# Optimization experiments

Hardware: AMD Instinct MI355X
Metric: run time of the kernel (lower is better)

The kernel has to match this reference:

```python
import jax, jax.numpy as jnp
import numpy as np

# Plain-RNN variant of RNNX (output_sizes=None): 2 stacked Elman layers,
# per layer: h' = tanh(Linear(concat(x, h))). batch_first=False -> Xt is [T, B, I].
T, B, I, H = 512, 128, 256, 512


def setup_inputs() -> dict:
    key = jax.random.key(0)
    k0, k1, k2, k3, k4 = jax.random.split(key, 5)
    stdv = 1.0 / np.sqrt(H)  # reset_parameters: uniform(-1/sqrt(hs), 1/sqrt(hs))
    return {
        "Xt": jax.random.normal(k0, (T, B, I), dtype=jnp.float32),
        "W1": jax.random.uniform(k1, (I + H, H), dtype=jnp.float32, minval=-stdv, maxval=stdv),
        "b1": jax.random.uniform(k2, (H,), dtype=jnp.float32, minval=-stdv, maxval=stdv),
        "W2": jax.random.uniform(k3, (H + H, H), dtype=jnp.float32, minval=-stdv, maxval=stdv),
        "b2": jax.random.uniform(k4, (H,), dtype=jnp.float32, minval=-stdv, maxval=stdv),
    }


def reference(Xt, W1, b1, W2, b2):
    # Xt: [T, B, I]; returns (out [T, B, H] stacked layer-2 outputs, hidden [2, B, H])
    Bsz = Xt.shape[1]
    Hd = W1.shape[1]
    h0 = (jnp.zeros((Bsz, Hd), Xt.dtype), jnp.zeros((Bsz, Hd), Xt.dtype))

    def step(h, x_t):
        h1, h2 = h
        y1 = jnp.tanh(jnp.concatenate([x_t, h1], axis=-1) @ W1 + b1)  # layer 1
        y2 = jnp.tanh(jnp.concatenate([y1, h2], axis=-1) @ W2 + b2)   # layer 2
        return (y1, y2), y2

    (h1f, h2f), out = jax.lax.scan(step, h0, Xt)
    hidden = jnp.stack([h1f, h2f], axis=0)  # [n_layers, B, H]
    return out, hidden
```

## Files before the change

kernel.cpp:

```cpp
#include <hip/hip_runtime.h>
#include <hip/hip_bf16.h>

#define TT 512
#define BB 128
#define II 256
#define HH 512

#define NGROUP 8
#define WPG    16
#define NWG    (NGROUP * WPG)

typedef __attribute__((ext_vector_type(8))) unsigned short ushort8;
typedef __attribute__((ext_vector_type(8))) __bf16         bf16x8;
typedef __attribute__((ext_vector_type(4))) float          float4v;
typedef unsigned long long u64;

union frag8 { ushort8 u; bf16x8 b; u64 q[2]; };

__device__ __forceinline__ unsigned short f2bf(float f) {
    union { float f; unsigned u; } v; v.f = f;
    return (unsigned short)((v.u + 0x7FFFu + ((v.u >> 16) & 1u)) >> 16);
}
__device__ __forceinline__ float bf2f(unsigned short h) {
    union { unsigned u; float f; } v; v.u = ((unsigned)h) << 16;
    return v.f;
}
__device__ __forceinline__ float tanh_fast(float x) {
    float e = __expf(2.0f * x);
    return 1.0f - 2.0f / (e + 1.0f);
}
__device__ __forceinline__ float4v mfma(bf16x8 a, bf16x8 b, float4v c) {
    return __builtin_amdgcn_mfma_f32_16x16x32_bf16(a, b, c, 0, 0, 0);
}
__device__ __forceinline__ u64 ald(const unsigned short* p) {
    return __hip_atomic_load((u64*)(void*)p, __ATOMIC_RELAXED, __HIP_MEMORY_SCOPE_AGENT);
}
__device__ __forceinline__ void ast(unsigned short* p, u64 v) {
    __hip_atomic_store((u64*)(void*)p, v, __ATOMIC_RELAXED, __HIP_MEMORY_SCOPE_AGENT);
}

__global__ __launch_bounds__(256, 1) void rnn_fused(
    const float* __restrict__ Xt,
    const float* __restrict__ W1,
    const float* __restrict__ b1,
    const float* __restrict__ W2,
    const float* __restrict__ b2,
    float* __restrict__ out,
    unsigned short* __restrict__ Ybuf,
    unsigned int* __restrict__ cnt)
{
    const int wg  = blockIdx.x;
    const int g   = wg & 7;
    const int j   = wg >> 3;
    const int tid = threadIdx.x;
    const int w   = tid >> 6;
    const int c   = w & 1;
    const int kh  = w >> 1;
    const int l   = tid & 63;
    const int lr  = l & 15;
    const int lq  = l >> 4;
    const int n0  = j * 32 + c * 16;
    const int row0 = g * 16;

    unsigned short* Y1 = Ybuf;
    unsigned short* Y2 = Ybuf + 2 * BB * HH;

    __shared__ float lp1[2][64][4];
    __shared__ float lp2[2][64][4];
    __shared__ __align__(8) unsigned short tr[4][16][20];

    frag8 w1h[12], w1l[12], w2h[16], w2l[16];
    const int kb1 = kh * 12, kb2 = kh * 16;
#pragma unroll
    for (int q = 0; q < 12; ++q)
#pragma unroll
        for (int e = 0; e < 8; ++e) {
            float v = W1[((kb1 + q) * 32 + lq * 8 + e) * HH + n0 + lr];
            unsigned short hi = f2bf(v);
            w1h[q].u[e] = hi;
            w1l[q].u[e] = f2bf(v - bf2f(hi));
        }
#pragma unroll
    for (int q = 0; q < 16; ++q)
#pragma unroll
        for (int e = 0; e < 8; ++e) {
            float v = W2[((kb2 + q) * 32 + lq * 8 + e) * HH + n0 + lr];
            unsigned short hi = f2bf(v);
            w2h[q].u[e] = hi;
            w2l[q].u[e] = f2bf(v - bf2f(hi));
        }
    const float bias1 = b1[n0 + lr];
    const float bias2 = b2[n0 + lr];

#pragma unroll 1
    for (int t = 0; t <= TT; ++t) {
        const int par = t & 1;
        const unsigned short* y1r = Y1 + (par ^ 1) * (BB * HH);
        const unsigned short* y2r = Y2 + par * (BB * HH);
        unsigned short* y1w = Y1 + par * (BB * HH);
        unsigned short* y2w = Y2 + (par ^ 1) * (BB * HH);

        frag8 a1[16], a2[16];
        if (kh == 0) {
#pragma unroll
            for (int q = 0; q < 16; ++q) {
                const unsigned short* p = y1r + (row0 + lr) * HH + q * 32 + lq * 8;
                a1[q].q[0] = ald(p); a1[q].q[1] = ald(p + 4);
            }
        } else {
#pragma unroll
            for (int q = 4; q < 16; ++q) {
                const unsigned short* p = y1r + (row0 + lr) * HH + q * 32 + lq * 8;
                a1[q].q[0] = ald(p); a1[q].q[1] = ald(p + 4);
            }
            if (t >= 1) {
#pragma unroll
                for (int q = 0; q < 16; ++q) {
                    const unsigned short* p = y2r + (row0 + lr) * HH + q * 32 + lq * 8;
                    a2[q].q[0] = ald(p); a2[q].q[1] = ald(p + 4);
                }
            }
        }

        float4v acc1  = {bias1, bias1, bias1, bias1};
        float4v acc1b = {0.f, 0.f, 0.f, 0.f};
        float4v acc2  = {bias2, bias2, bias2, bias2};
        float4v acc2b = {0.f, 0.f, 0.f, 0.f};
        if (kh == 0) acc2 = acc1b;
        else         acc1 = acc1b;

        if (kh == 0) {
            if (t < TT) {
#pragma unroll
                for (int q = 0; q < 8; ++q) {
                    const float* xp = Xt + ((size_t)t * BB + row0 + lr) * II + q * 32 + lq * 8;
                    float4v x0 = *(const float4v*)xp;
                    float4v x1 = *(const float4v*)(xp + 4);
                    frag8 ax;
#pragma unroll
                    for (int e = 0; e < 4; ++e) { ax.u[e] = f2bf(x0[e]); ax.u[4 + e] = f2bf(x1[e]); }
                    acc1  = mfma(ax.b, w1h[q].b, acc1);
                    acc1b = mfma(ax.b, w1l[q].b, acc1b);
                }
#pragma unroll
                for (int q = 0; q < 4; ++q) {
                    acc1  = mfma(a1[q].b, w1h[8 + q].b, acc1);
                    acc1b = mfma(a1[q].b, w1l[8 + q].b, acc1b);
                }
            }
            if (t >= 1) {
#pragma unroll
                for (int q = 0; q < 16; ++q) {
                    acc2  = mfma(a1[q].b, w2h[q].b, acc2);
                    acc2b = mfma(a1[q].b, w2l[q].b, acc2b);
                }
            }
        } else {
            if (t < TT) {
#pragma unroll
                for (int q = 0; q < 12; ++q) {
                    acc1  = mfma(a1[4 + q].b, w1h[q].b, acc1);
                    acc1b = mfma(a1[4 + q].b, w1l[q].b, acc1b);
                }
            }
            if (t >= 1) {
#pragma unroll
                for (int q = 0; q < 16; ++q) {
                    acc2  = mfma(a2[q].b, w2h[q].b, acc2);
                    acc2b = mfma(a2[q].b, w2l[q].b, acc2b);
                }
            }
        }

        if (kh == 1 && t < TT)  *(float4v*)&lp1[c][l][0] = acc1 + acc1b;
        if (kh == 0 && t >= 1)  *(float4v*)&lp2[c][l][0] = acc2 + acc2b;
        __syncthreads();

        float yout[4];
        if (kh == 0 && t < TT) {
            float4v p = *(const float4v*)&lp1[c][l][0];
#pragma unroll
            for (int i = 0; i < 4; ++i) {
                float y = tanh_fast(acc1[i] + acc1b[i] + p[i]);
                tr[w][lq * 4 + i][lr] = f2bf(y);
                yout[i] = y;
            }
        }
        if (kh == 1 && t >= 1) {
            float4v p = *(const float4v*)&lp2[c][l][0];
#pragma unroll
            for (int i = 0; i < 4; ++i) {
                float y = tanh_fast(acc2[i] + acc2b[i] + p[i]);
                tr[w][lq * 4 + i][lr] = f2bf(y);
                yout[i] = y;
            }
        }
        {
            const int row = l & 15, ch = l >> 4;
            if (kh == 0 && t < TT) {
                u64 v = *(const u64*)&tr[w][row][ch * 4];
                ast(y1w + (row0 + row) * HH + n0 + ch * 4, v);
            }
            if (kh == 1 && t >= 1) {
                u64 v = *(const u64*)&tr[w][row][ch * 4];
                ast(y2w + (row0 + row) * HH + n0 + ch * 4, v);
            }
        }

        asm volatile("s_waitcnt vmcnt(0) lgkmcnt(0)" ::: "memory");
        __syncthreads();

        if (t < TT && tid == 0)
            __hip_atomic_fetch_add(cnt + g * 1024 + t, 1u, __ATOMIC_RELAXED,
                                   __HIP_MEMORY_SCOPE_AGENT);

        if (kh == 1 && t >= 1) {
#pragma unroll
            for (int i = 0; i < 4; ++i) {
                const int r = row0 + lq * 4 + i;
                __builtin_nontemporal_store(yout[i], &out[((size_t)(t - 1) * BB + r) * HH + n0 + lr]);
                if (t == TT)
                    __builtin_nontemporal_store(yout[i],
                        &out[(size_t)TT * BB * HH + (size_t)BB * HH + (size_t)r * HH + n0 + lr]);
            }
        }
        if (kh == 0 && t == TT - 1) {
#pragma unroll
            for (int i = 0; i < 4; ++i) {
                const int r = row0 + lq * 4 + i;
                __builtin_nontemporal_store(yout[i],
                    &out[(size_t)TT * BB * HH + (size_t)r * HH + n0 + lr]);
            }
        }

        if (t < TT) {
            if (tid == 0) {
                while (__hip_atomic_load(cnt + g * 1024 + t, __ATOMIC_RELAXED,
                                         __HIP_MEMORY_SCOPE_AGENT) < WPG)
                    __builtin_amdgcn_s_sleep(1);
            }
            __syncthreads();
        }
    }
}

extern "C" void kernel_launch(void* const* d_in, const int* in_sizes, int n_in,
                              void* d_out, int out_size, void* d_ws, size_t ws_size,
                              hipStream_t stream) {
    const float* Xt = (const float*)d_in[0];
    const float* W1 = (const float*)d_in[1];
    const float* b1 = (const float*)d_in[2];
    const float* W2 = (const float*)d_in[3];
    const float* b2 = (const float*)d_in[4];
    float* out = (float*)d_out;

    unsigned short* Ybuf = (unsigned short*)d_ws;
    unsigned int*   cnt  = (unsigned int*)((char*)d_ws + 4 * BB * HH * 2);
    size_t zero_bytes = (size_t)4 * BB * HH * 2 + (size_t)NGROUP * 1024 * 4;

    hipMemsetAsync(d_ws, 0, zero_bytes, stream);
    hipLaunchKernelGGL(rnn_fused, dim3(NWG), dim3(256), 0, stream,
                       Xt, W1, b1, W2, b2, out, Ybuf, cnt);
}
```

Measured before the change: 5.468 ms.

## Replace group counter barrier with per-wave flags and prefetch X into LDS

Each step previously ended with a workgroup barrier, a single atomic counter increment per group and a thread-0 spin. That is replaced by per-wave step flags: every wave publishes its own flag and then polls all flags in its group with one wavefront vote, which removes the extra __syncthreads and the serialized spin. The next timestep's X rows are prefetched into a double-buffered LDS area with asynchronous global-to-LDS loads, so X reads come off the critical path. Layer-2 output stores are also deferred by one step so they leave the recurrence tail. The risks are busy-wait traffic on shared flags and subtle cross-wave ordering of the LDS buffers, which now relies on the flag protocol.

```diff
diff --git a/kernel.cpp b/kernel.cpp
--- a/kernel.cpp
+++ b/kernel.cpp
@@ -1,5 +1,4 @@
 #include <hip/hip_runtime.h>
-#include <hip/hip_bf16.h>
 
 #define TT 512
 #define BB 128
@@ -33,10 +32,16 @@
     return __builtin_amdgcn_mfma_f32_16x16x32_bf16(a, b, c, 0, 0, 0);
 }
 __device__ __forceinline__ u64 ald(const unsigned short* p) {
-    return __hip_atomic_load((u64*)(void*)p, __ATOMIC_RELAXED, __HIP_MEMORY_SCOPE_AGENT);
+    return __hip_atomic_load((const u64*)(const void*)p, __ATOMIC_RELAXED, __HIP_MEMORY_SCOPE_AGENT);
 }
 __device__ __forceinline__ void ast(unsigned short* p, u64 v) {
     __hip_atomic_store((u64*)(void*)p, v, __ATOMIC_RELAXED, __HIP_MEMORY_SCOPE_AGENT);
+}
+__device__ __forceinline__ unsigned ald32(const unsigned* p) {
+    return __hip_atomic_load(p, __ATOMIC_RELAXED, __HIP_MEMORY_SCOPE_AGENT);
+}
+__device__ __forceinline__ void ast32(unsigned* p, unsigned v) {
+    __hip_atomic_store(p, v, __ATOMIC_RELAXED, __HIP_MEMORY_SCOPE_AGENT);
 }
 
 __global__ __launch_bounds__(256, 1) void rnn_fused(
@@ -47,7 +52,7 @@
     const float* __restrict__ b2,
     float* __restrict__ out,
     unsigned short* __restrict__ Ybuf,
-    unsigned int* __restrict__ cnt)
+    unsigned* __restrict__ slots)
 {
     const int wg  = blockIdx.x;
     const int g   = wg & 7;
@@ -61,10 +66,12 @@
     const int lq  = l >> 4;
     const int n0  = j * 32 + c * 16;
     const int row0 = g * 16;
+    const int mywave = j * 4 + w;
 
     unsigned short* Y1 = Ybuf;
     unsigned short* Y2 = Ybuf + 2 * BB * HH;
 
+    __shared__ float xlds[2][16][256];
     __shared__ float lp1[2][64][4];
     __shared__ float lp2[2][64][4];
     __shared__ __align__(8) unsigned short tr[4][16][20];
@@ -91,6 +98,20 @@
         }
     const float bias1 = b1[n0 + lr];
     const float bias2 = b2[n0 + lr];
+
+    if (w < 2) {
+#pragma unroll
+        for (int i = 0; i < 8; ++i) {
+            int ci = w * 8 + i;
+            const float* gs = Xt + ((size_t)0 * BB + row0 + ci) * II + l * 4;
+            __builtin_amdgcn_global_load_lds(
+                (const __attribute__((address_space(1))) void*)gs,
+                (__attribute__((address_space(3))) void*)&xlds[0][ci][0], 16, 0, 0);
+        }
+    }
+    __syncthreads();
+
+    float yprev[4] = {0.f, 0.f, 0.f, 0.f};
 
 #pragma unroll 1
     for (int t = 0; t <= TT; ++t) {
@@ -100,6 +121,15 @@
         unsigned short* y1w = Y1 + par * (BB * HH);
         unsigned short* y2w = Y2 + (par ^ 1) * (BB * HH);
 
+        if (kh == 1 && t >= 2) {
+#pragma unroll
+            for (int i = 0; i < 4; ++i) {
+                const int r = row0 + lq * 4 + i;
+                __builtin_nontemporal_store(yprev[i],
+                    &out[((size_t)(t - 2) * BB + r) * HH + n0 + lr]);
+            }
+        }
+
         frag8 a1[16], a2[16];
         if (kh == 0) {
 #pragma unroll
@@ -122,20 +152,31 @@
             }
         }
 
-        float4v acc1  = {bias1, bias1, bias1, bias1};
+        if (w < 2 && t < TT - 1) {
+#pragma unroll
+            for (int i = 0; i < 8; ++i) {
+                int ci = w * 8 + i;
+                const float* gs = Xt + ((size_t)(t + 1) * BB + row0 + ci) * II + l * 4;
+                __builtin_amdgcn_global_load_lds(
+                    (const __attribute__((address_space(1))) void*)gs,
+                    (__attribute__((address_space(3))) void*)&xlds[par ^ 1][ci][0], 16, 0, 0);
+            }
+        }
+
+        float4v acc1  = {0.f, 0.f, 0.f, 0.f};
         float4v acc1b = {0.f, 0.f, 0.f, 0.f};
-        float4v acc2  = {bias2, bias2, bias2, bias2};
+        float4v acc2  = {0.f, 0.f, 0.f, 0.f};
         float4v acc2b = {0.f, 0.f, 0.f, 0.f};
-        if (kh == 0) acc2 = acc1b;
-        else         acc1 = acc1b;
+        if (kh == 0) { acc1[0] = acc1[1] = acc1[2] = acc1[3] = bias1; }
+        else         { acc2[0] = acc2[1] = acc2[2] = acc2[3] = bias2; }
 
         if (kh == 0) {
             if (t < TT) {
 #pragma unroll
                 for (int q = 0; q < 8; ++q) {
-                    const float* xp = Xt + ((size_t)t * BB + row0 + lr) * II + q * 32 + lq * 8;
-                    float4v x0 = *(const float4v*)xp;
-                    float4v x1 = *(const float4v*)(xp + 4);
+                    const float* xr = &xlds[par][lr][q * 32 + lq * 8];
+                    float4v x0 = *(const float4v*)xr;
+                    float4v x1 = *(const float4v*)(xr + 4);
                     frag8 ax;
 #pragma unroll
                     for (int e = 0; e < 4; ++e) { ax.u[e] = f2bf(x0[e]); ax.u[4 + e] = f2bf(x1[e]); }
@@ -176,15 +217,21 @@
         if (kh == 0 && t >= 1)  *(float4v*)&lp2[c][l][0] = acc2 + acc2b;
         __syncthreads();
 
-        float yout[4];
         if (kh == 0 && t < TT) {
             float4v p = *(const float4v*)&lp1[c][l][0];
+            float yv[4];
 #pragma unroll
             for (int i = 0; i < 4; ++i) {
-                float y = tanh_fast(acc1[i] + acc1b[i] + p[i]);
-                tr[w][lq * 4 + i][lr] = f2bf(y);
-                yout[i] = y;
-            }
+                yv[i] = tanh_fast(acc1[i] + acc1b[i] + p[i]);
+                tr[w][lq * 4 + i][lr] = f2bf(yv[i]);
+            }
+            if (t == TT - 1) {
+#pragma unroll
+                for (int i = 0; i < 4; ++i)
+                    out[(size_t)TT * BB * HH + (size_t)(row0 + lq * 4 + i) * HH + n0 + lr] = yv[i];
+            }
+            u64 v = *(const u64*)&tr[w][lr][lq * 4];
+            ast(y1w + (row0 + lr) * HH + n0 + lq * 4, v);
         }
         if (kh == 1 && t >= 1) {
             float4v p = *(const float4v*)&lp2[c][l][0];
@@ -192,54 +239,27 @@
             for (int i = 0; i < 4; ++i) {
                 float y = tanh_fast(acc2[i] + acc2b[i] + p[i]);
                 tr[w][lq * 4 + i][lr] = f2bf(y);
-                yout[i] = y;
-            }
-        }
-        {
-            const int row = l & 15, ch = l >> 4;
-            if (kh == 0 && t < TT) {
-                u64 v = *(const u64*)&tr[w][row][ch * 4];
-                ast(y1w + (row0 + row) * HH + n0 + ch * 4, v);
-            }
-            if (kh == 1 && t >= 1) {
-                u64 v = *(const u64*)&tr[w][row][ch * 4];
-                ast(y2w + (row0 + row) * HH + n0 + ch * 4, v);
-            }
-        }
-
-        asm volatile("s_waitcnt vmcnt(0) lgkmcnt(0)" ::: "memory");
-        __syncthreads();
-
-        if (t < TT && tid == 0)
-            __hip_atomic_fetch_add(cnt + g * 1024 + t, 1u, __ATOMIC_RELAXED,
-                                   __HIP_MEMORY_SCOPE_AGENT);
-
-        if (kh == 1 && t >= 1) {
-#pragma unroll
-            for (int i = 0; i < 4; ++i) {
-                const int r = row0 + lq * 4 + i;
-                __builtin_nontemporal_store(yout[i], &out[((size_t)(t - 1) * BB + r) * HH + n0 + lr]);
-                if (t == TT)
-                    __builtin_nontemporal_store(yout[i],
-                        &out[(size_t)TT * BB * HH + (size_t)BB * HH + (size_t)r * HH + n0 + lr]);
-            }
-        }
-        if (kh == 0 && t == TT - 1) {
-#pragma unroll
-            for (int i = 0; i < 4; ++i) {
-                const int r = row0 + lq * 4 + i;
-                __builtin_nontemporal_store(yout[i],
-                    &out[(size_t)TT * BB * HH + (size_t)r * HH + n0 + lr]);
-            }
+                yprev[i] = y;
+            }
+            u64 v = *(const u64*)&tr[w][lr][lq * 4];
+            ast(y2w + (row0 + lr) * HH + n0 + lq * 4, v);
         }
 
         if (t < TT) {
-            if (tid == 0) {
-                while (__hip_atomic_load(cnt + g * 1024 + t, __ATOMIC_RELAXED,
-                                         __HIP_MEMORY_SCOPE_AGENT) < WPG)
-                    __builtin_amdgcn_s_sleep(1);
-            }
-            __syncthreads();
+            asm volatile("s_waitcnt vmcnt(0)" ::: "memory");
+            if (l == 0) ast32(slots + g * 64 + mywave, (unsigned)(t + 1));
+            const unsigned* pp = slots + g * 64 + l;
+            while (!__all(ald32(pp) > (unsigned)t)) { }
+            __builtin_amdgcn_fence(__ATOMIC_ACQUIRE, "workgroup");
+        }
+    }
+
+    if (kh == 1) {
+#pragma unroll
+        for (int i = 0; i < 4; ++i) {
+            const int r = row0 + lq * 4 + i;
+            out[((size_t)(TT - 1) * BB + r) * HH + n0 + lr] = yprev[i];
+            out[(size_t)TT * BB * HH + (size_t)BB * HH + (size_t)r * HH + n0 + lr] = yprev[i];
         }
     }
 }
@@ -254,11 +274,11 @@
     const float* b2 = (const float*)d_in[4];
     float* out = (float*)d_out;
 
-    unsigned short* Ybuf = (unsigned short*)d_ws;
-    unsigned int*   cnt  = (unsigned int*)((char*)d_ws + 4 * BB * HH * 2);
-    size_t zero_bytes = (size_t)4 * BB * HH * 2 + (size_t)NGROUP * 1024 * 4;
+    unsigned short* Ybuf  = (unsigned short*)d_ws;
+    unsigned*       slots = (unsigned*)((char*)d_ws + 4 * BB * HH * 2);
+    size_t zero_bytes = (size_t)4 * BB * HH * 2 + (size_t)NGROUP * 64 * 4;
 
     hipMemsetAsync(d_ws, 0, zero_bytes, stream);
     hipLaunchKernelGGL(rnn_fused, dim3(NWG), dim3(256), 0, stream,
-                       Xt, W1, b1, W2, b2, out, Ybuf, cnt);
-}
+                       Xt, W1, b1, W2, b2, out, Ybuf, slots);
+}
```

Measured after the change: 7.015 ms. +28.3%, slower.
